# Performance work log

Measured on AMD Instinct MI355X. Metric: run time of the kernel, lower is better.

The kernel has to match this reference:

```python
import jax, jax.numpy as jnp
import numpy as np

B, N, D, C = 256, 200000, 128, 1000


def _l2_normalize(v, axis=-1, eps=1e-12):
    # matches torch F.normalize(p=2): v / max(||v||, eps)
    norm = jnp.sqrt(jnp.sum(v * v, axis=axis, keepdims=True))
    return v / jnp.maximum(norm, eps)


def setup_inputs() -> dict:
    key = jax.random.key(0)
    k1, k2, k3 = jax.random.split(key, 3)
    x = jax.random.normal(k1, (B, D), dtype=jnp.float32)
    index_embeddings = jax.random.normal(k2, (N, D), dtype=jnp.float32)
    class_labels = jax.random.randint(k3, (N,), 0, C, dtype=jnp.int32)
    return {
        "x": x,
        "index_embeddings": index_embeddings,
        "class_labels": class_labels,
        "num_classes": C,
    }


def reference(x, index_embeddings, class_labels, num_classes):
    # backbone output flattened -> embeddings [B, D]; L2-normalize (queries and index,
    # index normalization happens in add_index_data in the original module)
    emb = _l2_normalize(x)
    idx_emb = _l2_normalize(index_embeddings)
    # cosine similarities [B, N]
    similarities = jnp.einsum('bd,nd->bn', emb, idx_emb)
    # per-class max reduction (replaces Python loop over classes):
    # segment-max over the index dimension keyed by class_labels -> [B, num_classes]
    logits = jax.ops.segment_max(
        similarities.T, class_labels, num_segments=num_classes,
        indices_are_sorted=False,
    ).T
    return logits
```

## Files before the change

kernel.cpp:

```cpp
#include <hip/hip_runtime.h>
#include <hip/hip_bf16.h>
#include <stdint.h>

#define D_ 128
#define NB 64
#define NINF (-__builtin_inff())

typedef float f32x4 __attribute__((ext_vector_type(4)));
typedef short bf16x8 __attribute__((ext_vector_type(8)));

__device__ inline unsigned short f2bf(float f){
  unsigned x = __float_as_uint(f);
  return (unsigned short)((x + 0x7FFFu + ((x >> 16) & 1u)) >> 16);
}
__device__ inline unsigned packbf(float a, float b){
  return (unsigned)f2bf(a) | ((unsigned)f2bf(b) << 16);
}
__device__ inline unsigned fkey(float v){
  unsigned b = __float_as_uint(v);
  return (b & 0x80000000u) ? ~b : (b | 0x80000000u);
}

__global__ void k_prep(const float* __restrict__ emb, const float* __restrict__ x,
                       unsigned short* __restrict__ nrmlin, unsigned short* __restrict__ xn,
                       unsigned* __restrict__ out_u, const int* __restrict__ lab,
                       unsigned* __restrict__ hist,
                       int N, int B, int C, int PN, int XB, int IB, int HB){
  const int bid = blockIdx.x;
  const int t = threadIdx.x;
  if (bid < PN + XB){
    const float* src; unsigned short* dst; int nrows; int r0;
    if (bid < PN){ src = emb; dst = nrmlin; nrows = N; r0 = bid * 64; }
    else         { src = x;   dst = xn;     nrows = B; r0 = (bid - PN) * 64; }
    int r = r0 + (t >> 2);
    if (r >= nrows) return;
    int j = t & 3;
    const f32x4* s4 = reinterpret_cast<const f32x4*>(src + (size_t)r * D_ + j * 32);
    f32x4 v[8];
    #pragma unroll
    for (int i = 0; i < 8; i++) v[i] = s4[i];
    float ss = 0.f;
    #pragma unroll
    for (int i = 0; i < 8; i++) ss += v[i][0]*v[i][0] + v[i][1]*v[i][1] + v[i][2]*v[i][2] + v[i][3]*v[i][3];
    ss += __shfl_xor(ss, 1); ss += __shfl_xor(ss, 2);
    float sc = 1.0f / fmaxf(sqrtf(ss), 1e-12f);
    unsigned o[16];
    #pragma unroll
    for (int i = 0; i < 8; i++){
      o[i*2]   = packbf(v[i][0]*sc, v[i][1]*sc);
      o[i*2+1] = packbf(v[i][2]*sc, v[i][3]*sc);
    }
    uint4* d4 = reinterpret_cast<uint4*>(dst + (size_t)r * D_ + j * 32);
    #pragma unroll
    for (int i = 0; i < 4; i++) d4[i] = make_uint4(o[i*4], o[i*4+1], o[i*4+2], o[i*4+3]);
  } else if (bid < PN + XB + IB){
    int i = (bid - PN - XB) * 256 + t;
    if (i < B * C) out_u[i] = 0x007FFFFFu;
  } else {
    int hb = bid - PN - XB - IB;
    __shared__ unsigned lh[1024];
    for (int c = t; c < 1024; c += 256) lh[c] = 0;
    __syncthreads();
    for (int i = hb * 256 + t; i < N; i += HB * 256) atomicAdd(&lh[lab[i]], 1u);
    __syncthreads();
    for (int c = t; c < C; c += 256){ unsigned v = lh[c]; if (v) atomicAdd(&hist[c], v); }
  }
}

__global__ void k_scan(const unsigned* __restrict__ hist, unsigned* __restrict__ cursor, int C){
  __shared__ unsigned s[1024];
  int t = threadIdx.x;
  unsigned v = (t < C) ? hist[t] : 0u;
  s[t] = v; __syncthreads();
  for (int off = 1; off < 1024; off <<= 1){
    unsigned u = (t >= off) ? s[t - off] : 0u;
    __syncthreads();
    s[t] += u;
    __syncthreads();
  }
  if (t < C) cursor[t] = s[t] - v;
}

__global__ void k_scatter(const int* __restrict__ lab, unsigned* __restrict__ cursor,
                          int* __restrict__ perm, int* __restrict__ slab, int N){
  for (int i = blockIdx.x * 256 + threadIdx.x; i < N; i += gridDim.x * 256){
    int c = lab[i];
    unsigned pos = atomicAdd(&cursor[c], 1u);
    perm[pos] = i;
    slab[pos] = c;
  }
}

__global__ __launch_bounds__(256, 3) void k_gemm(
    const unsigned short* __restrict__ nrmlin,
    const unsigned short* __restrict__ xn,
    const int* __restrict__ perm, const int* __restrict__ slab,
    unsigned* __restrict__ out_u, int N, int C){
  __shared__ __align__(16) unsigned short Ab[NB * D_];
  const int t = threadIdx.x, w = t >> 6, lane = t & 63, lr = lane & 15, lg = lane >> 4;
  const int rowbase = blockIdx.x * NB;

  int rb = rowbase + lane;
  int myc = slab[rb < N ? rb : (N - 1)];

  #pragma unroll
  for (int i = 0; i < 4; i++){
    int gr = rowbase + i * 16 + lr; if (gr > N - 1) gr = N - 1;
    int g = perm[gr];
    const char* src = (const char*)nrmlin + (size_t)g * 256 + ((w * 4 + lg) << 4);
    char* dst = (char*)Ab + (w + i * 4) * 1024 + lane * 16;
    __builtin_amdgcn_global_load_lds(
        (const __attribute__((address_space(1))) unsigned int*)src,
        (__attribute__((address_space(3))) unsigned int*)dst, 16, 0, 0);
  }

  bf16x8 bf[4][4];
  #pragma unroll
  for (int ni = 0; ni < 4; ni++)
    #pragma unroll
    for (int kk = 0; kk < 4; kk++)
      bf[ni][kk] = *reinterpret_cast<const bf16x8*>(
          xn + (size_t)(w * 64 + ni * 16 + lr) * D_ + kk * 32 + lg * 8);

  int nx = __shfl_down(myc, 1);
  unsigned long long bmask = __ballot(lane < 63 && myc != nx);
  int c0 = __shfl(myc, 0);

  __syncthreads();

  f32x4 acc[4][4];
  #pragma unroll
  for (int mi = 0; mi < 4; mi++)
    #pragma unroll
    for (int ni = 0; ni < 4; ni++)
      acc[mi][ni] = (f32x4){0.f, 0.f, 0.f, 0.f};

  #pragma unroll
  for (int mi = 0; mi < 4; mi++)
    #pragma unroll
    for (int kk = 0; kk < 4; kk++){
      bf16x8 af = *reinterpret_cast<const bf16x8*>(&Ab[(mi * 4 + kk) * 512 + lane * 8]);
      #pragma unroll
      for (int ni = 0; ni < 4; ni++)
        acc[mi][ni] = __builtin_amdgcn_mfma_f32_16x16x32_bf16(af, bf[ni][kk], acc[mi][ni], 0, 0, 0);
    }

  if (bmask == 0ULL){
    float m0=NINF, m1=NINF, m2=NINF, m3=NINF;
    #pragma unroll
    for (int mi = 0; mi < 4; mi++)
      #pragma unroll
      for (int rg = 0; rg < 4; rg++){
        m0 = fmaxf(m0, acc[mi][0][rg]);
        m1 = fmaxf(m1, acc[mi][1][rg]);
        m2 = fmaxf(m2, acc[mi][2][rg]);
        m3 = fmaxf(m3, acc[mi][3][rg]);
      }
    m0 = fmaxf(m0, __shfl_xor(m0, 16)); m0 = fmaxf(m0, __shfl_xor(m0, 32));
    m1 = fmaxf(m1, __shfl_xor(m1, 16)); m1 = fmaxf(m1, __shfl_xor(m1, 32));
    m2 = fmaxf(m2, __shfl_xor(m2, 16)); m2 = fmaxf(m2, __shfl_xor(m2, 32));
    m3 = fmaxf(m3, __shfl_xor(m3, 16)); m3 = fmaxf(m3, __shfl_xor(m3, 32));
    float mv = (lg < 2) ? ((lg == 0) ? m0 : m1) : ((lg == 2) ? m2 : m3);
    atomicMax(&out_u[(size_t)t * C + c0], fkey(mv));
  } else {
    int a = 0;
    unsigned long long mm = bmask;
    for (;;){
      int e = mm ? (__builtin_ctzll(mm) + 1) : 64;
      int cls = __shfl(myc, a);
      float m0=NINF, m1=NINF, m2=NINF, m3=NINF;
      #pragma unroll
      for (int mi = 0; mi < 4; mi++)
        #pragma unroll
        for (int rg = 0; rg < 4; rg++){
          int row = mi * 16 + lg * 4 + rg;
          bool in = (row >= a) && (row < e);
          m0 = in ? fmaxf(m0, acc[mi][0][rg]) : m0;
          m1 = in ? fmaxf(m1, acc[mi][1][rg]) : m1;
          m2 = in ? fmaxf(m2, acc[mi][2][rg]) : m2;
          m3 = in ? fmaxf(m3, acc[mi][3][rg]) : m3;
        }
      m0 = fmaxf(m0, __shfl_xor(m0, 16)); m0 = fmaxf(m0, __shfl_xor(m0, 32));
      m1 = fmaxf(m1, __shfl_xor(m1, 16)); m1 = fmaxf(m1, __shfl_xor(m1, 32));
      m2 = fmaxf(m2, __shfl_xor(m2, 16)); m2 = fmaxf(m2, __shfl_xor(m2, 32));
      m3 = fmaxf(m3, __shfl_xor(m3, 16)); m3 = fmaxf(m3, __shfl_xor(m3, 32));
      float mv = (lg < 2) ? ((lg == 0) ? m0 : m1) : ((lg == 2) ? m2 : m3);
      atomicMax(&out_u[(size_t)t * C + cls], fkey(mv));
      if (e >= 64) break;
      a = e; mm &= mm - 1;
    }
  }
}

struct __align__(16) GSm {
  unsigned short A[NB * 136];
  float sims[16 * 257];
  float scale[NB];
  int rowid[NB];
  int clab[NB];
};

__global__ __launch_bounds__(256, 2) void k_gemm_gather(
    const float* __restrict__ emb, const unsigned short* __restrict__ xn,
    const int* __restrict__ perm, const int* __restrict__ slab,
    unsigned* __restrict__ out_u, int N, int C){
  __shared__ GSm sm;
  const int t = threadIdx.x;
  const int base = blockIdx.x * NB;
  if (t < NB){
    int p = base + t; if (p > N - 1) p = N - 1;
    sm.rowid[t] = perm[p];
    sm.clab[t]  = slab[p];
  }
  __syncthreads();
  {
    int r = t >> 2, j = t & 3;
    const float4* src = reinterpret_cast<const float4*>(emb + (long)sm.rowid[r] * D_ + j * 32);
    float4 v[8];
    #pragma unroll
    for (int i = 0; i < 8; i++) v[i] = src[i];
    float ss = 0.f;
    #pragma unroll
    for (int i = 0; i < 8; i++) ss += v[i].x*v[i].x + v[i].y*v[i].y + v[i].z*v[i].z + v[i].w*v[i].w;
    ss += __shfl_xor(ss, 1); ss += __shfl_xor(ss, 2);
    sm.scale[r] = 1.0f / fmaxf(sqrtf(ss), 1e-12f);
    unsigned* dst = reinterpret_cast<unsigned*>(&sm.A[r * 136 + j * 32]);
    #pragma unroll
    for (int i = 0; i < 8; i++){
      dst[i * 2]     = packbf(v[i].x, v[i].y);
      dst[i * 2 + 1] = packbf(v[i].z, v[i].w);
    }
  }
  const int w = t >> 6, lane = t & 63;
  const int lr = lane & 15, lg = lane >> 4;
  bf16x8 bfr[4][4];
  #pragma unroll
  for (int ni = 0; ni < 4; ni++)
    #pragma unroll
    for (int kk = 0; kk < 4; kk++)
      bfr[ni][kk] = *reinterpret_cast<const bf16x8*>(
          xn + (size_t)(w * 64 + ni * 16 + lr) * D_ + kk * 32 + lg * 8);
  f32x4 acc[4][4];
  #pragma unroll
  for (int mi = 0; mi < 4; mi++)
    #pragma unroll
    for (int ni = 0; ni < 4; ni++)
      acc[mi][ni] = (f32x4){0.f, 0.f, 0.f, 0.f};
  __syncthreads();
  #pragma unroll
  for (int mi = 0; mi < 4; mi++)
    #pragma unroll
    for (int kk = 0; kk < 4; kk++){
      bf16x8 af = *reinterpret_cast<const bf16x8*>(&sm.A[(mi * 16 + lr) * 136 + kk * 32 + lg * 8]);
      #pragma unroll
      for (int ni = 0; ni < 4; ni++)
        acc[mi][ni] = __builtin_amdgcn_mfma_f32_16x16x32_bf16(af, bfr[ni][kk], acc[mi][ni], 0, 0, 0);
    }
  int cur = -1; float rm = 0.f;
  for (int mi = 0; mi < 4; mi++){
    __syncthreads();
    #pragma unroll
    for (int ni = 0; ni < 4; ni++)
      #pragma unroll
      for (int rg = 0; rg < 4; rg++){
        int r16 = lg * 4 + rg;
        sm.sims[r16 * 257 + w * 64 + ni * 16 + lr] = acc[mi][ni][rg] * sm.scale[mi * 16 + r16];
      }
    __syncthreads();
    #pragma unroll
    for (int r16 = 0; r16 < 16; r16++){
      int c = sm.clab[mi * 16 + r16];
      float v = sm.sims[r16 * 257 + t];
      if (c != cur){
        if (cur >= 0) atomicMax(&out_u[(size_t)t * C + cur], fkey(rm));
        cur = c; rm = v;
      } else rm = fmaxf(rm, v);
    }
  }
  atomicMax(&out_u[(size_t)t * C + cur], fkey(rm));
}

__global__ void k_finalize(unsigned* __restrict__ o, int n){
  int i = blockIdx.x * 256 + threadIdx.x;
  if (i < n){
    unsigned k = o[i];
    o[i] = (k & 0x80000000u) ? (k & 0x7FFFFFFFu) : ~k;
  }
}

extern "C" void kernel_launch(void* const* d_in, const int* in_sizes, int n_in,
                              void* d_out, int out_size, void* d_ws, size_t ws_size,
                              hipStream_t stream){
  const float* x   = (const float*)d_in[0];
  const float* emb = (const float*)d_in[1];
  const int*   lab = (const int*)d_in[2];
  const int B = in_sizes[0] / D_;
  const int N = in_sizes[1] / D_;
  const int C = out_size / B;

  const int PNfull = (N + 63) / 64;
  const int XB = (B + 63) / 64;
  const int IB = (B * C + 255) / 256;
  const int HB = 208;

  char* ws = (char*)d_ws;
  size_t off = 0;
  unsigned short* xn = (unsigned short*)(ws); off += ((size_t)B * D_ * 2 + 255) & ~(size_t)255;
  unsigned* hist   = (unsigned*)(ws + off); off += 4096;
  unsigned* cursor = (unsigned*)(ws + off); off += 4096;
  size_t narr = ((size_t)N * 4 + 255) & ~(size_t)255;
  int* perm   = (int*)(ws + off); off += narr;
  int* slab   = (int*)(ws + off); off += narr;
  unsigned short* nrmlin = (unsigned short*)(ws + off);
  size_t need = off + (size_t)PNfull * NB * D_ * 2;
  const bool fast = (ws_size >= need);
  const int PN = fast ? PNfull : 0;

  hipMemsetAsync(hist, 0, 4096, stream);
  k_prep<<<PN + XB + IB + HB, 256, 0, stream>>>(emb, x, nrmlin, xn, (unsigned*)d_out,
                                                lab, hist, N, B, C, PN, XB, IB, HB);
  k_scan<<<1, 1024, 0, stream>>>(hist, cursor, C);
  k_scatter<<<208, 256, 0, stream>>>(lab, cursor, perm, slab, N);
  if (fast){
    k_gemm<<<PNfull, 256, 0, stream>>>(nrmlin, xn, perm, slab, (unsigned*)d_out, N, C);
  } else {
    k_gemm_gather<<<PNfull, 256, 0, stream>>>(emb, xn, perm, slab, (unsigned*)d_out, N, C);
  }
  k_finalize<<<IB, 256, 0, stream>>>((unsigned*)d_out, B * C);
}
```

Before: 292.4 us.

## Assign one block per class and drop atomic segment-max and output init/finalize

The fast path now launches one block per class. Each block walks that class's sorted row range in 64-row chunks, double-buffered in LDS via global_load_lds, keeps a running max in registers, and writes the float result directly. This removes the output init pass, the atomicMax traffic to the output and the finalize kernel. In exchange the work is split by class rather than evenly by rows, so load balance depends on class sizes (about 200 rows, roughly 4 chunks each). Partial last chunks are handled by clamping to the class's last row, and the LDS footprint is doubled with occupancy lowered to 2.

```diff
diff --git a/kernel.cpp b/kernel.cpp
--- a/kernel.cpp
+++ b/kernel.cpp
@@ -23,9 +23,8 @@
 
 __global__ void k_prep(const float* __restrict__ emb, const float* __restrict__ x,
                        unsigned short* __restrict__ nrmlin, unsigned short* __restrict__ xn,
-                       unsigned* __restrict__ out_u, const int* __restrict__ lab,
-                       unsigned* __restrict__ hist,
-                       int N, int B, int C, int PN, int XB, int IB, int HB){
+                       const int* __restrict__ lab, unsigned* __restrict__ hist,
+                       int N, int B, int C, int PN, int XB, int HB){
   const int bid = blockIdx.x;
   const int t = threadIdx.x;
   if (bid < PN + XB){
@@ -53,11 +52,8 @@
     uint4* d4 = reinterpret_cast<uint4*>(dst + (size_t)r * D_ + j * 32);
     #pragma unroll
     for (int i = 0; i < 4; i++) d4[i] = make_uint4(o[i*4], o[i*4+1], o[i*4+2], o[i*4+3]);
-  } else if (bid < PN + XB + IB){
-    int i = (bid - PN - XB) * 256 + t;
-    if (i < B * C) out_u[i] = 0x007FFFFFu;
   } else {
-    int hb = bid - PN - XB - IB;
+    int hb = bid - PN - XB;
     __shared__ unsigned lh[1024];
     for (int c = t; c < 1024; c += 256) lh[c] = 0;
     __syncthreads();
@@ -67,7 +63,8 @@
   }
 }
 
-__global__ void k_scan(const unsigned* __restrict__ hist, unsigned* __restrict__ cursor, int C){
+__global__ void k_scan(const unsigned* __restrict__ hist, unsigned* __restrict__ cursor,
+                       unsigned* __restrict__ cbase, int C){
   __shared__ unsigned s[1024];
   int t = threadIdx.x;
   unsigned v = (t < C) ? hist[t] : 0u;
@@ -78,7 +75,7 @@
     s[t] += u;
     __syncthreads();
   }
-  if (t < C) cursor[t] = s[t] - v;
+  if (t < C){ unsigned e = s[t] - v; cursor[t] = e; cbase[t] = e; }
 }
 
 __global__ void k_scatter(const int* __restrict__ lab, unsigned* __restrict__ cursor,
@@ -91,28 +88,46 @@
   }
 }
 
-__global__ __launch_bounds__(256, 3) void k_gemm(
+__global__ __launch_bounds__(256, 2) void k_gemm_cls(
     const unsigned short* __restrict__ nrmlin,
     const unsigned short* __restrict__ xn,
-    const int* __restrict__ perm, const int* __restrict__ slab,
-    unsigned* __restrict__ out_u, int N, int C){
-  __shared__ __align__(16) unsigned short Ab[NB * D_];
+    const int* __restrict__ perm,
+    const unsigned* __restrict__ cbase, const unsigned* __restrict__ hist,
+    float* __restrict__ out, int N, int C){
+  const int c = blockIdx.x;
   const int t = threadIdx.x, w = t >> 6, lane = t & 63, lr = lane & 15, lg = lane >> 4;
-  const int rowbase = blockIdx.x * NB;
-
-  int rb = rowbase + lane;
-  int myc = slab[rb < N ? rb : (N - 1)];
-
-  #pragma unroll
-  for (int i = 0; i < 4; i++){
-    int gr = rowbase + i * 16 + lr; if (gr > N - 1) gr = N - 1;
-    int g = perm[gr];
-    const char* src = (const char*)nrmlin + (size_t)g * 256 + ((w * 4 + lg) << 4);
-    char* dst = (char*)Ab + (w + i * 4) * 1024 + lane * 16;
-    __builtin_amdgcn_global_load_lds(
-        (const __attribute__((address_space(1))) unsigned int*)src,
-        (__attribute__((address_space(3))) unsigned int*)dst, 16, 0, 0);
-  }
+  const int nrows = (int)hist[c];
+  if (nrows == 0){ out[(size_t)t * C + c] = NINF; return; }
+  const int base = (int)cbase[c];
+  const int last = base + nrows - 1;
+  const int chunks = (nrows + NB - 1) >> 6;
+
+  __shared__ __align__(16) unsigned short Ab[2][NB * D_];
+
+  auto rid_load = [&](int ci, int (&r)[4]){
+    int cc = ci < chunks ? ci : chunks - 1;
+    #pragma unroll
+    for (int i = 0; i < 4; i++){
+      int gr = base + cc * NB + i * 16 + lr;
+      if (gr > last) gr = last;
+      r[i] = perm[gr];
+    }
+  };
+  auto stage = [&](int bb, const int (&r)[4]){
+    #pragma unroll
+    for (int i = 0; i < 4; i++){
+      const char* src = (const char*)nrmlin + (size_t)r[i] * 256 + ((w * 4 + lg) << 4);
+      char* dst = (char*)(&Ab[bb][0]) + (w + i * 4) * 1024 + lane * 16;
+      __builtin_amdgcn_global_load_lds(
+          (const __attribute__((address_space(1))) unsigned int*)src,
+          (__attribute__((address_space(3))) unsigned int*)dst, 16, 0, 0);
+    }
+  };
+
+  int ridN[4];
+  rid_load(0, ridN);
+  stage(0, ridN);
+  rid_load(1, ridN);
 
   bf16x8 bf[4][4];
   #pragma unroll
@@ -122,74 +137,55 @@
       bf[ni][kk] = *reinterpret_cast<const bf16x8*>(
           xn + (size_t)(w * 64 + ni * 16 + lr) * D_ + kk * 32 + lg * 8);
 
-  int nx = __shfl_down(myc, 1);
-  unsigned long long bmask = __ballot(lane < 63 && myc != nx);
-  int c0 = __shfl(myc, 0);
-
-  __syncthreads();
-
-  f32x4 acc[4][4];
-  #pragma unroll
-  for (int mi = 0; mi < 4; mi++)
-    #pragma unroll
-    for (int ni = 0; ni < 4; ni++)
-      acc[mi][ni] = (f32x4){0.f, 0.f, 0.f, 0.f};
-
-  #pragma unroll
-  for (int mi = 0; mi < 4; mi++)
-    #pragma unroll
-    for (int kk = 0; kk < 4; kk++){
-      bf16x8 af = *reinterpret_cast<const bf16x8*>(&Ab[(mi * 4 + kk) * 512 + lane * 8]);
+  float M0 = NINF, M1 = NINF, M2 = NINF, M3 = NINF;
+
+  for (int ci = 0; ci < chunks; ++ci){
+    const int b = ci & 1;
+    stage(b ^ 1, ridN);
+    rid_load(ci + 2, ridN);
+    __builtin_amdgcn_s_barrier();
+
+    f32x4 acc[4][4];
+    #pragma unroll
+    for (int mi = 0; mi < 4; mi++)
       #pragma unroll
       for (int ni = 0; ni < 4; ni++)
-        acc[mi][ni] = __builtin_amdgcn_mfma_f32_16x16x32_bf16(af, bf[ni][kk], acc[mi][ni], 0, 0, 0);
-    }
-
-  if (bmask == 0ULL){
-    float m0=NINF, m1=NINF, m2=NINF, m3=NINF;
+        acc[mi][ni] = (f32x4){0.f, 0.f, 0.f, 0.f};
+
     #pragma unroll
     for (int mi = 0; mi < 4; mi++)
       #pragma unroll
+      for (int kk = 0; kk < 4; kk++){
+        bf16x8 af = *reinterpret_cast<const bf16x8*>(&Ab[b][(mi * 4 + kk) * 512 + lane * 8]);
+        #pragma unroll
+        for (int ni = 0; ni < 4; ni++)
+          acc[mi][ni] = __builtin_amdgcn_mfma_f32_16x16x32_bf16(af, bf[ni][kk], acc[mi][ni], 0, 0, 0);
+      }
+    __builtin_amdgcn_s_barrier();
+
+    #pragma unroll
+    for (int mi = 0; mi < 4; mi++)
+      #pragma unroll
       for (int rg = 0; rg < 4; rg++){
-        m0 = fmaxf(m0, acc[mi][0][rg]);
-        m1 = fmaxf(m1, acc[mi][1][rg]);
-        m2 = fmaxf(m2, acc[mi][2][rg]);
-        m3 = fmaxf(m3, acc[mi][3][rg]);
+        M0 = fmaxf(M0, acc[mi][0][rg]);
+        M1 = fmaxf(M1, acc[mi][1][rg]);
+        M2 = fmaxf(M2, acc[mi][2][rg]);
+        M3 = fmaxf(M3, acc[mi][3][rg]);
       }
-    m0 = fmaxf(m0, __shfl_xor(m0, 16)); m0 = fmaxf(m0, __shfl_xor(m0, 32));
-    m1 = fmaxf(m1, __shfl_xor(m1, 16)); m1 = fmaxf(m1, __shfl_xor(m1, 32));
-    m2 = fmaxf(m2, __shfl_xor(m2, 16)); m2 = fmaxf(m2, __shfl_xor(m2, 32));
-    m3 = fmaxf(m3, __shfl_xor(m3, 16)); m3 = fmaxf(m3, __shfl_xor(m3, 32));
-    float mv = (lg < 2) ? ((lg == 0) ? m0 : m1) : ((lg == 2) ? m2 : m3);
-    atomicMax(&out_u[(size_t)t * C + c0], fkey(mv));
-  } else {
-    int a = 0;
-    unsigned long long mm = bmask;
-    for (;;){
-      int e = mm ? (__builtin_ctzll(mm) + 1) : 64;
-      int cls = __shfl(myc, a);
-      float m0=NINF, m1=NINF, m2=NINF, m3=NINF;
-      #pragma unroll
-      for (int mi = 0; mi < 4; mi++)
-        #pragma unroll
-        for (int rg = 0; rg < 4; rg++){
-          int row = mi * 16 + lg * 4 + rg;
-          bool in = (row >= a) && (row < e);
-          m0 = in ? fmaxf(m0, acc[mi][0][rg]) : m0;
-          m1 = in ? fmaxf(m1, acc[mi][1][rg]) : m1;
-          m2 = in ? fmaxf(m2, acc[mi][2][rg]) : m2;
-          m3 = in ? fmaxf(m3, acc[mi][3][rg]) : m3;
-        }
-      m0 = fmaxf(m0, __shfl_xor(m0, 16)); m0 = fmaxf(m0, __shfl_xor(m0, 32));
-      m1 = fmaxf(m1, __shfl_xor(m1, 16)); m1 = fmaxf(m1, __shfl_xor(m1, 32));
-      m2 = fmaxf(m2, __shfl_xor(m2, 16)); m2 = fmaxf(m2, __shfl_xor(m2, 32));
-      m3 = fmaxf(m3, __shfl_xor(m3, 16)); m3 = fmaxf(m3, __shfl_xor(m3, 32));
-      float mv = (lg < 2) ? ((lg == 0) ? m0 : m1) : ((lg == 2) ? m2 : m3);
-      atomicMax(&out_u[(size_t)t * C + cls], fkey(mv));
-      if (e >= 64) break;
-      a = e; mm &= mm - 1;
-    }
-  }
+  }
+  asm volatile("s_waitcnt vmcnt(0)" ::: "memory");
+
+  M0 = fmaxf(M0, __shfl_xor(M0, 16)); M0 = fmaxf(M0, __shfl_xor(M0, 32));
+  M1 = fmaxf(M1, __shfl_xor(M1, 16)); M1 = fmaxf(M1, __shfl_xor(M1, 32));
+  M2 = fmaxf(M2, __shfl_xor(M2, 16)); M2 = fmaxf(M2, __shfl_xor(M2, 32));
+  M3 = fmaxf(M3, __shfl_xor(M3, 16)); M3 = fmaxf(M3, __shfl_xor(M3, 32));
+  float mv = (lg < 2) ? ((lg == 0) ? M0 : M1) : ((lg == 2) ? M2 : M3);
+  out[(size_t)t * C + c] = mv;
+}
+
+__global__ void k_init_out(unsigned* __restrict__ o, int n){
+  int i = blockIdx.x * 256 + threadIdx.x;
+  if (i < n) o[i] = 0x007FFFFFu;
 }
 
 struct __align__(16) GSm {
@@ -269,11 +265,11 @@
     __syncthreads();
     #pragma unroll
     for (int r16 = 0; r16 < 16; r16++){
-      int c = sm.clab[mi * 16 + r16];
+      int cc = sm.clab[mi * 16 + r16];
       float v = sm.sims[r16 * 257 + t];
-      if (c != cur){
+      if (cc != cur){
         if (cur >= 0) atomicMax(&out_u[(size_t)t * C + cur], fkey(rm));
-        cur = c; rm = v;
+        cur = cc; rm = v;
       } else rm = fmaxf(rm, v);
     }
   }
@@ -300,7 +296,6 @@
 
   const int PNfull = (N + 63) / 64;
   const int XB = (B + 63) / 64;
-  const int IB = (B * C + 255) / 256;
   const int HB = 208;
 
   char* ws = (char*)d_ws;
@@ -308,23 +303,27 @@
   unsigned short* xn = (unsigned short*)(ws); off += ((size_t)B * D_ * 2 + 255) & ~(size_t)255;
   unsigned* hist   = (unsigned*)(ws + off); off += 4096;
   unsigned* cursor = (unsigned*)(ws + off); off += 4096;
+  unsigned* cbase  = (unsigned*)(ws + off); off += 4096;
   size_t narr = ((size_t)N * 4 + 255) & ~(size_t)255;
   int* perm   = (int*)(ws + off); off += narr;
   int* slab   = (int*)(ws + off); off += narr;
   unsigned short* nrmlin = (unsigned short*)(ws + off);
-  size_t need = off + (size_t)PNfull * NB * D_ * 2;
+  size_t need = off + (size_t)N * D_ * 2;
   const bool fast = (ws_size >= need);
   const int PN = fast ? PNfull : 0;
 
   hipMemsetAsync(hist, 0, 4096, stream);
-  k_prep<<<PN + XB + IB + HB, 256, 0, stream>>>(emb, x, nrmlin, xn, (unsigned*)d_out,
-                                                lab, hist, N, B, C, PN, XB, IB, HB);
-  k_scan<<<1, 1024, 0, stream>>>(hist, cursor, C);
+  k_prep<<<PN + XB + HB, 256, 0, stream>>>(emb, x, nrmlin, xn, lab, hist,
+                                           N, B, C, PN, XB, HB);
+  k_scan<<<1, 1024, 0, stream>>>(hist, cursor, cbase, C);
   k_scatter<<<208, 256, 0, stream>>>(lab, cursor, perm, slab, N);
   if (fast){
-    k_gemm<<<PNfull, 256, 0, stream>>>(nrmlin, xn, perm, slab, (unsigned*)d_out, N, C);
+    k_gemm_cls<<<C, 256, 0, stream>>>(nrmlin, xn, perm, cbase, hist,
+                                      (float*)d_out, N, C);
   } else {
+    const int IB = (B * C + 255) / 256;
+    k_init_out<<<IB, 256, 0, stream>>>((unsigned*)d_out, B * C);
     k_gemm_gather<<<PNfull, 256, 0, stream>>>(emb, xn, perm, slab, (unsigned*)d_out, N, C);
-  }
-  k_finalize<<<IB, 256, 0, stream>>>((unsigned*)d_out, B * C);
-}
+    k_finalize<<<IB, 256, 0, stream>>>((unsigned*)d_out, B * C);
+  }
+}
```

Measured after the change: 243.1 us. 1.2x faster.
